# Kernel optimization log

Hardware: AMD Instinct MI355X
Metric: run time of the kernel (lower is better)

The kernel has to match this reference:

```python
import jax, jax.numpy as jnp
import numpy as np

DEPTH = 10
WIDTH = 128
DIM = 2
N = 1_048_576


def setup_inputs() -> dict:
    key = jax.random.key(0)
    ks = jax.random.split(key, 14)
    x = jax.random.normal(ks[0], (N, DIM), jnp.float32)

    # Orthogonal init for the invertible 1x1 convs (QR of a random matrix),
    # matching Invertible1x1Conv.__init__.
    rng = np.random.default_rng(0)
    conv_w = np.stack([np.linalg.qr(rng.standard_normal((DIM, DIM)))[0]
                       for _ in range(DEPTH)]).astype(np.float32)

    def nrm(k, shape, sc=0.1):
        return sc * jax.random.normal(k, shape, jnp.float32)

    return dict(
        x=x,
        an_scale=jnp.exp(nrm(ks[1], (DEPTH, DIM))),          # outer actnorm, positive
        an_bias=nrm(ks[2], (DEPTH, DIM)),
        conv_w=jnp.asarray(conv_w),                           # [D, 2, 2]
        fc1_w=nrm(ks[3], (DEPTH, WIDTH, DIM // 2), 1.0),      # Linear(1, 128)
        fc1_b=nrm(ks[4], (DEPTH, WIDTH)),
        an1_scale=jnp.exp(nrm(ks[5], (DEPTH, WIDTH))),
        an1_bias=nrm(ks[6], (DEPTH, WIDTH)),
        fc2_w=nrm(ks[7], (DEPTH, WIDTH, WIDTH)),              # Linear(128, 128)
        fc2_b=nrm(ks[8], (DEPTH, WIDTH)),
        an2_scale=jnp.exp(nrm(ks[9], (DEPTH, WIDTH))),
        an2_bias=nrm(ks[10], (DEPTH, WIDTH)),
        fc3_w=nrm(ks[11], (DEPTH, DIM, WIDTH)),               # Linear(128, 2)
        fc3_b=nrm(ks[12], (DEPTH, DIM)),
        log_scale_factor=nrm(ks[13], (DEPTH, DIM)),
    )


def reference(x, an_scale, an_bias, conv_w, fc1_w, fc1_b, an1_scale, an1_bias,
              fc2_w, fc2_b, an2_scale, an2_bias, fc3_w, fc3_b, log_scale_factor):
    z = x
    logdet = jnp.zeros((x.shape[0],), x.dtype)
    half = DIM // 2
    for i in range(DEPTH):  # fixed depth=10, structurally distinct params
        # --- Actnorm ---
        z = (z - an_bias[i]) / an_scale[i]
        logdet = logdet - jnp.sum(jnp.log(jnp.abs(an_scale[i])))
        # --- Invertible 1x1 conv ---
        logdet = logdet + jnp.linalg.slogdet(conv_w[i])[1]
        z = z @ conv_w[i].T
        # --- Affine coupling (inner actnorms are already initialized) ---
        z_a, z_b = z[:, :half], z[:, half:]
        h = jax.nn.relu((z_b @ fc1_w[i].T + fc1_b[i] - an1_bias[i]) / an1_scale[i])
        h = jax.nn.relu((h @ fc2_w[i].T + fc2_b[i] - an2_bias[i]) / an2_scale[i])
        h = (h @ fc3_w[i].T + fc3_b[i]) * jnp.exp(log_scale_factor[i])  # [N, 2]
        t = h[:, 0::2]                         # [N, 1]
        s = jax.nn.sigmoid(h[:, 1::2] + 2.0)   # [N, 1]
        z = jnp.concatenate([s * z_a + t, z_b], axis=1)
        logdet = logdet + jnp.sum(jnp.log(s), axis=1)
    return z, logdet
```

## Files before the change

kernel.cpp:

```cpp
#include <hip/hip_runtime.h>
#include <math.h>


constexpr int kDepth = 10;
constexpr int kWidth = 128;
constexpr float kVMin = -24.0f;
constexpr float kVMax =  24.0f;

__global__ void prep_kernel(
    const float* __restrict__ an_scale, const float* __restrict__ an_bias,
    const float* __restrict__ conv_w,
    const float* __restrict__ fc1_w, const float* __restrict__ fc1_b,
    const float* __restrict__ an1_scale, const float* __restrict__ an1_bias,
    const float* __restrict__ fc2_w, const float* __restrict__ fc2_b,
    const float* __restrict__ an2_scale, const float* __restrict__ an2_bias,
    const float* __restrict__ fc3_b, const float* __restrict__ lsf,
    float* __restrict__ meta, float* __restrict__ kv,
    float* __restrict__ CG, float* __restrict__ CB)
{
  __shared__ float sWT[128 * 129];
  __shared__ float sVs[128], sG[128], sB[128];
  __shared__ float sGs[128], sBs[128];
  __shared__ int   sOrd[128];

  const int l = blockIdx.x;
  const int t = threadIdx.x;

  const float* wl = fc2_w + (size_t)l * kWidth * kWidth;
#pragma unroll 8
  for (int fi = t; fi < 128 * 128; fi += 256) {
    const int k = fi >> 7, j = fi & 127;
    sWT[j * 129 + k] = wl[fi];
  }

  if (t < 128) {
    const float s1 = an1_scale[l*kWidth + t];
    const float g = fc1_w[l*kWidth + t] / s1;
    const float b = (fc1_b[l*kWidth + t] - an1_bias[l*kWidth + t]) / s1;
    float vs, sg;
    if (g > 0.0f)      { vs = -b / g; sg =  1.0f; }
    else if (g < 0.0f) { vs = -b / g; sg = -1.0f; }
    else               { vs = (b > 0.0f) ? -1e30f : 1e30f; sg = (b > 0.0f) ? 1.0f : 0.0f; }
    sG[t] = g; sB[t] = b; sVs[t] = vs;
    sGs[t] = sg * g; sBs[t] = sg * b;
  }
  __syncthreads();

  if (t < 128) {
    const float my = sVs[t];
    int r = 0;
    const float4* vs4 = (const float4*)sVs;
#pragma unroll
    for (int i4 = 0; i4 < 32; ++i4) {
      float4 o = vs4[i4];
      const int ib = i4 * 4;
      r += (o.x < my) || (o.x == my && ib + 0 < t);
      r += (o.y < my) || (o.y == my && ib + 1 < t);
      r += (o.z < my) || (o.z == my && ib + 2 < t);
      r += (o.w < my) || (o.w == my && ib + 3 < t);
    }
    sOrd[r] = t;
  }
  __syncthreads();

  if (t < 128) {
    kv[l*128 + t] = sVs[sOrd[t]];

    float cg = 0.0f;
    float cb = fc2_b[l*kWidth + t] - an2_bias[l*kWidth + t];
    const float4* g4 = (const float4*)sG;
    const float4* b4 = (const float4*)sB;
#pragma unroll
    for (int j4 = 0; j4 < 32; ++j4) {
      float4 G = g4[j4], B = b4[j4];
      const int j = j4 * 4;
      float w0 = sWT[(j + 0) * 129 + t];
      float w1 = sWT[(j + 1) * 129 + t];
      float w2 = sWT[(j + 2) * 129 + t];
      float w3 = sWT[(j + 3) * 129 + t];
      if (G.x < 0.0f) { cg = fmaf(G.x, w0, cg); cb = fmaf(B.x, w0, cb); }
      if (G.y < 0.0f) { cg = fmaf(G.y, w1, cg); cb = fmaf(B.y, w1, cb); }
      if (G.z < 0.0f) { cg = fmaf(G.z, w2, cg); cb = fmaf(B.z, w2, cb); }
      if (G.w < 0.0f) { cg = fmaf(G.w, w3, cg); cb = fmaf(B.w, w3, cb); }
    }

    const size_t base = (size_t)l * 129 * 128;
    int4 J = ((const int4*)sOrd)[0];
    float w0 = sWT[J.x * 129 + t];
    float w1 = sWT[J.y * 129 + t];
    float w2 = sWT[J.z * 129 + t];
    float w3 = sWT[J.w * 129 + t];
#pragma unroll 1
    for (int c = 0; c < 32; ++c) {
      const int4 Jc = J;
      const float v0 = w0, v1 = w1, v2 = w2, v3 = w3;
      if (c + 1 < 32) {
        J = ((const int4*)sOrd)[c + 1];
        w0 = sWT[J.x * 129 + t];
        w1 = sWT[J.y * 129 + t];
        w2 = sWT[J.z * 129 + t];
        w3 = sWT[J.w * 129 + t];
      }
      const int p = c * 4;
      CG[base + (size_t)(p + 0) * 128 + t] = cg;
      CB[base + (size_t)(p + 0) * 128 + t] = cb;
      cg = fmaf(sGs[Jc.x], v0, cg); cb = fmaf(sBs[Jc.x], v0, cb);
      CG[base + (size_t)(p + 1) * 128 + t] = cg;
      CB[base + (size_t)(p + 1) * 128 + t] = cb;
      cg = fmaf(sGs[Jc.y], v1, cg); cb = fmaf(sBs[Jc.y], v1, cb);
      CG[base + (size_t)(p + 2) * 128 + t] = cg;
      CB[base + (size_t)(p + 2) * 128 + t] = cb;
      cg = fmaf(sGs[Jc.z], v2, cg); cb = fmaf(sBs[Jc.z], v2, cb);
      CG[base + (size_t)(p + 3) * 128 + t] = cg;
      CB[base + (size_t)(p + 3) * 128 + t] = cb;
      cg = fmaf(sGs[Jc.w], v3, cg); cb = fmaf(sBs[Jc.w], v3, cb);
    }
    CG[base + (size_t)128 * 128 + t] = cg;
    CB[base + (size_t)128 * 128 + t] = cb;
  }

  if (t == 0) {
    meta[16 + l*4 + 0] = expf(lsf[l*2 + 0]);
    meta[16 + l*4 + 1] = expf(lsf[l*2 + 1]);
    meta[16 + l*4 + 2] = fc3_b[l*2 + 0];
    meta[16 + l*4 + 3] = fc3_b[l*2 + 1];

    const float sx = an_scale[l*2+0], sy = an_scale[l*2+1];
    const float bx = an_bias[l*2+0],  by = an_bias[l*2+1];
    const float* cw = conv_w + l*4;
    const float m00 = cw[0]/sx, m01 = cw[1]/sy;
    const float m10 = cw[2]/sx, m11 = cw[3]/sy;
    meta[64 + l*8 + 0] = m00;
    meta[64 + l*8 + 1] = m01;
    meta[64 + l*8 + 2] = m10;
    meta[64 + l*8 + 3] = m11;
    meta[64 + l*8 + 4] = -(m00*bx + m01*by);
    meta[64 + l*8 + 5] = -(m10*bx + m11*by);
  }
  if (l == 0 && t == 0) {
    float cst = 0.0f;
    for (int i = 0; i < kDepth; ++i) {
      cst -= logf(fabsf(an_scale[i*2+0]));
      cst -= logf(fabsf(an_scale[i*2+1]));
      const float* cw = conv_w + i * 4;
      float det = cw[0]*cw[3] - cw[1]*cw[2];
      cst += logf(fabsf(det));
    }
    meta[0] = cst;
  }
}

__global__ __launch_bounds__(256) void table_kernel(
    const float* __restrict__ an2_scale,
    const float* __restrict__ fc3_w,
    const float* __restrict__ meta, const float* __restrict__ kv,
    const float* __restrict__ CG, const float* __restrict__ CB,
    int tabN, float4* __restrict__ tab)
{
  __shared__ float sKz[128], sKw[128], sKv[128];
  __shared__ int   sP[64];

  const int bpl   = tabN >> 6;
  const int l     = blockIdx.x / bpl;
  const int node0 = (blockIdx.x % bpl) * 64;
  const int t     = threadIdx.x;
  const float dv  = (kVMax - kVMin) / (float)(tabN - 1);

  if (t < 128) {
    const float si = 1.0f / an2_scale[l*kWidth + t];
    sKz[t] = fc3_w[l*2*kWidth + t] * si;
    sKw[t] = fc3_w[l*2*kWidth + kWidth + t] * si;
    sKv[t] = kv[l*128 + t];
  }
  __syncthreads();

  if (t < 64) {
    const float v = kVMin + dv * (float)(node0 + t);
    int p = 0;
    const float4* kv4 = (const float4*)sKv;
#pragma unroll
    for (int m = 0; m < 32; ++m) {
      float4 K = kv4[m];
      p += (K.x < v) + (K.y < v) + (K.z < v) + (K.w < v);
    }
    sP[t] = p;
  }
  __syncthreads();

  const int node = t >> 2, kq = t & 3;
  const int p = sP[node];
  const float v = kVMin + dv * (float)(node0 + node);

  const float4* cg4 = (const float4*)(CG + ((size_t)l*129 + p) * 128 + kq*32);
  const float4* cb4 = (const float4*)(CB + ((size_t)l*129 + p) * 128 + kq*32);
  const float4* kz4 = (const float4*)sKz + kq*8;
  const float4* kw4 = (const float4*)sKw + kq*8;

  float o0 = 0.f, o1 = 0.f, p0 = 0.f, p1 = 0.f;
#pragma unroll
  for (int c = 0; c < 8; ++c) {
    float4 G = cg4[c], B = cb4[c], Z = kz4[c], W = kw4[c];
    float raw, h, dd;
    raw = fmaf(v, G.x, B.x); h = fmaxf(raw, 0.f); dd = (raw > 0.f) ? G.x : 0.f;
    o0 = fmaf(h, Z.x, o0); o1 = fmaf(h, W.x, o1); p0 = fmaf(dd, Z.x, p0); p1 = fmaf(dd, W.x, p1);
    raw = fmaf(v, G.y, B.y); h = fmaxf(raw, 0.f); dd = (raw > 0.f) ? G.y : 0.f;
    o0 = fmaf(h, Z.y, o0); o1 = fmaf(h, W.y, o1); p0 = fmaf(dd, Z.y, p0); p1 = fmaf(dd, W.y, p1);
    raw = fmaf(v, G.z, B.z); h = fmaxf(raw, 0.f); dd = (raw > 0.f) ? G.z : 0.f;
    o0 = fmaf(h, Z.z, o0); o1 = fmaf(h, W.z, o1); p0 = fmaf(dd, Z.z, p0); p1 = fmaf(dd, W.z, p1);
    raw = fmaf(v, G.w, B.w); h = fmaxf(raw, 0.f); dd = (raw > 0.f) ? G.w : 0.f;
    o0 = fmaf(h, Z.w, o0); o1 = fmaf(h, W.w, o1); p0 = fmaf(dd, Z.w, p0); p1 = fmaf(dd, W.w, p1);
  }

  o0 += __shfl_xor(o0, 1); o0 += __shfl_xor(o0, 2);
  o1 += __shfl_xor(o1, 1); o1 += __shfl_xor(o1, 2);
  p0 += __shfl_xor(p0, 1); p0 += __shfl_xor(p0, 2);
  p1 += __shfl_xor(p1, 1); p1 += __shfl_xor(p1, 2);

  if (kq == 0) {
    const float E0  = meta[16 + l*4 + 0];
    const float E1  = meta[16 + l*4 + 1];
    const float b30 = meta[16 + l*4 + 2];
    const float b31 = meta[16 + l*4 + 3];
    tab[(size_t)l * tabN + node0 + node] =
        make_float4((o0 + b30) * E0, p0 * E0, (o1 + b31) * E1, p1 * E1);
  }
}

__global__ __launch_bounds__(1024) void flow_apply_kernel(
    const float* __restrict__ x,
    const float4* __restrict__ tab, const float* __restrict__ meta,
    int tabN,
    float* __restrict__ out_z, float* __restrict__ out_ld, int n)
{
  __shared__ float2 sTU[2][1024];
  __shared__ float2 sDT[2][1024];

  const int t = threadIdx.x;
  const int base = blockIdx.x * 4096;

  int   sid[4];
  bool  ok[4];
  float2 z[4];
  float ldv[4];
  const float ldc = meta[0];
#pragma unroll
  for (int c = 0; c < 4; ++c) {
    sid[c] = base + c * 1024 + t;
    ok[c] = sid[c] < n;
    z[c] = ok[c] ? reinterpret_cast<const float2*>(x)[sid[c]] : make_float2(0.f, 0.f);
    ldv[c] = ldc;
  }

  const float dv = (kVMax - kVMin) / (float)(tabN - 1);
  const float inv_dv = (float)(tabN - 1) / (kVMax - kVMin);
  const float offv = -kVMin * inv_dv;
  const float qmax = (float)(tabN - 1);
  constexpr float kLog2e = 1.44269504088896340736f;
  constexpr float kLn2   = 0.69314718055994530942f;

  if (t < tabN) {
    float4 e = tab[t];
    sTU[0][t] = make_float2(e.x, e.z);
    sDT[0][t] = make_float2(e.y, e.w);
  }
  __syncthreads();

  int cur = 0;
#pragma unroll 1
  for (int i = 0; i < kDepth; ++i) {
    float4 en = make_float4(0.f, 0.f, 0.f, 0.f);
    if (i + 1 < kDepth && t < tabN)
      en = tab[(size_t)(i + 1) * tabN + t];

    const float m00 = meta[64 + i*8 + 0], m01 = meta[64 + i*8 + 1];
    const float m10 = meta[64 + i*8 + 2], m11 = meta[64 + i*8 + 3];
    const float q0  = meta[64 + i*8 + 4], q1  = meta[64 + i*8 + 5];
    const float2* tu = sTU[cur];
    const float2* dt = sDT[cur];

#pragma unroll
    for (int c = 0; c < 4; ++c) {
      const float na = fmaf(m00, z[c].x, fmaf(m01, z[c].y, q0));
      const float nb = fmaf(m10, z[c].x, fmaf(m11, z[c].y, q1));
      float xq = fmaf(nb, inv_dv, offv);
      xq = fminf(fmaxf(xq, 0.0f), qmax);
      const int qn = (int)(xq + 0.5f);
      const float2 e  = tu[qn];
      const float2 de = dt[qn];
      const float vn = fmaf((float)qn, dv, kVMin);
      const float f = nb - vn;
      const float tt = fmaf(f, de.x, e.x);
      const float uu = fmaf(f, de.y, e.y);
      const float arg = uu + 2.0f;
      const float ev = __builtin_amdgcn_exp2f(arg * -kLog2e);
      const float den = 1.0f + ev;
      const float s = __builtin_amdgcn_rcpf(den);
      ldv[c] = fmaf(-kLn2, __builtin_amdgcn_logf(den), ldv[c]);
      z[c].x = fmaf(s, na, tt);
      z[c].y = nb;
    }

    __syncthreads();
    if (i + 1 < kDepth && t < tabN) {
      sTU[cur ^ 1][t] = make_float2(en.x, en.z);
      sDT[cur ^ 1][t] = make_float2(en.y, en.w);
    }
    __syncthreads();
    cur ^= 1;
  }

#pragma unroll
  for (int c = 0; c < 4; ++c) {
    if (ok[c]) {
      reinterpret_cast<float2*>(out_z)[sid[c]] = z[c];
      out_ld[sid[c]] = ldv[c];
    }
  }
}

extern "C" void kernel_launch(void* const* d_in, const int* in_sizes, int n_in,
                              void* d_out, int out_size, void* d_ws, size_t ws_size,
                              hipStream_t stream) {
  const float* x         = (const float*)d_in[0];
  const float* an_scale  = (const float*)d_in[1];
  const float* an_bias   = (const float*)d_in[2];
  const float* conv_w    = (const float*)d_in[3];
  const float* fc1_w     = (const float*)d_in[4];
  const float* fc1_b     = (const float*)d_in[5];
  const float* an1_scale = (const float*)d_in[6];
  const float* an1_bias  = (const float*)d_in[7];
  const float* fc2_w     = (const float*)d_in[8];
  const float* fc2_b     = (const float*)d_in[9];
  const float* an2_scale = (const float*)d_in[10];
  const float* an2_bias  = (const float*)d_in[11];
  const float* fc3_w     = (const float*)d_in[12];
  const float* fc3_b     = (const float*)d_in[13];
  const float* lsf       = (const float*)d_in[14];

  const int n = in_sizes[0] / 2;

  const size_t metaF = 256, kvF = (size_t)kDepth * 128;
  const size_t cF = (size_t)kDepth * 129 * 128;
  const size_t headF = metaF + kvF + 2 * cF;
  int tabN = 1024;
  while (tabN > 256 &&
         headF * 4 + (size_t)kDepth * tabN * sizeof(float4) > ws_size) {
    tabN >>= 1;
  }
  float* meta = (float*)d_ws;
  float* kv   = meta + metaF;
  float* CG   = kv + kvF;
  float* CB   = CG + cF;
  float4* tab = (float4*)(CB + cF);

  prep_kernel<<<kDepth, 256, 0, stream>>>(
      an_scale, an_bias, conv_w, fc1_w, fc1_b, an1_scale, an1_bias,
      fc2_w, fc2_b, an2_scale, an2_bias, fc3_b, lsf,
      meta, kv, CG, CB);

  table_kernel<<<kDepth * (tabN / 64), 256, 0, stream>>>(
      an2_scale, fc3_w, meta, kv, CG, CB, tabN, tab);

  const int blocks = (n + 4095) / 4096;
  flow_apply_kernel<<<blocks, 1024, 0, stream>>>(
      x, tab, meta, tabN, (float*)d_out, (float*)d_out + (size_t)2 * n, n);
}
```

Before: 45.32 us.

## Preload all layer tables into LDS with bf16-packed slopes, drop per-layer barriers

Each block now loads every depth's lookup table into shared memory once at the start, instead of double-buffering one table per layer with two barriers per layer. To fit everything in LDS, the default table resolution drops from 1024 to 512 entries, and the two slope values are packed as bf16 into a single 32-bit word. This removes the per-layer synchronisation and the staggered global loads. The cost is a coarser piecewise-linear approximation and reduced slope precision, which could hurt accuracy, plus a larger LDS footprint per block.

Result: faster. 40.38 us (-10.9%).

```diff
diff --git a/kernel.cpp b/kernel.cpp
--- a/kernel.cpp
+++ b/kernel.cpp
@@ -226,17 +226,31 @@
   }
 }
 
+__device__ __forceinline__ unsigned int pack_bf16(float a, float b) {
+  unsigned int ua = __float_as_uint(a);
+  unsigned int ub = __float_as_uint(b);
+  ua = (ua + 0x7FFFu + ((ua >> 16) & 1u)) >> 16;
+  ub = (ub + 0x7FFFu + ((ub >> 16) & 1u)) >> 16;
+  return ua | (ub << 16);
+}
+
 __global__ __launch_bounds__(1024) void flow_apply_kernel(
     const float* __restrict__ x,
     const float4* __restrict__ tab, const float* __restrict__ meta,
     int tabN,
     float* __restrict__ out_z, float* __restrict__ out_ld, int n)
 {
-  __shared__ float2 sTU[2][1024];
-  __shared__ float2 sDT[2][1024];
+  __shared__ float2       sTU[kDepth * 512];
+  __shared__ unsigned int sPK[kDepth * 512];
 
   const int t = threadIdx.x;
   const int base = blockIdx.x * 4096;
+
+  for (int j = t; j < kDepth * tabN; j += 1024) {
+    float4 e = tab[j];
+    sTU[j] = make_float2(e.x, e.z);
+    sPK[j] = pack_bf16(e.y, e.w);
+  }
 
   int   sid[4];
   bool  ok[4];
@@ -258,25 +272,15 @@
   constexpr float kLog2e = 1.44269504088896340736f;
   constexpr float kLn2   = 0.69314718055994530942f;
 
-  if (t < tabN) {
-    float4 e = tab[t];
-    sTU[0][t] = make_float2(e.x, e.z);
-    sDT[0][t] = make_float2(e.y, e.w);
-  }
-  __syncthreads();
-
-  int cur = 0;
+  __syncthreads();
+
 #pragma unroll 1
   for (int i = 0; i < kDepth; ++i) {
-    float4 en = make_float4(0.f, 0.f, 0.f, 0.f);
-    if (i + 1 < kDepth && t < tabN)
-      en = tab[(size_t)(i + 1) * tabN + t];
-
     const float m00 = meta[64 + i*8 + 0], m01 = meta[64 + i*8 + 1];
     const float m10 = meta[64 + i*8 + 2], m11 = meta[64 + i*8 + 3];
     const float q0  = meta[64 + i*8 + 4], q1  = meta[64 + i*8 + 5];
-    const float2* tu = sTU[cur];
-    const float2* dt = sDT[cur];
+    const float2* tu = sTU + i * tabN;
+    const unsigned int* pk = sPK + i * tabN;
 
 #pragma unroll
     for (int c = 0; c < 4; ++c) {
@@ -285,12 +289,14 @@
       float xq = fmaf(nb, inv_dv, offv);
       xq = fminf(fmaxf(xq, 0.0f), qmax);
       const int qn = (int)(xq + 0.5f);
-      const float2 e  = tu[qn];
-      const float2 de = dt[qn];
+      const float2 e = tu[qn];
+      const unsigned int d = pk[qn];
+      const float dt = __uint_as_float(d << 16);
+      const float du = __uint_as_float(d & 0xFFFF0000u);
       const float vn = fmaf((float)qn, dv, kVMin);
       const float f = nb - vn;
-      const float tt = fmaf(f, de.x, e.x);
-      const float uu = fmaf(f, de.y, e.y);
+      const float tt = fmaf(f, dt, e.x);
+      const float uu = fmaf(f, du, e.y);
       const float arg = uu + 2.0f;
       const float ev = __builtin_amdgcn_exp2f(arg * -kLog2e);
       const float den = 1.0f + ev;
@@ -299,14 +305,6 @@
       z[c].x = fmaf(s, na, tt);
       z[c].y = nb;
     }
-
-    __syncthreads();
-    if (i + 1 < kDepth && t < tabN) {
-      sTU[cur ^ 1][t] = make_float2(en.x, en.z);
-      sDT[cur ^ 1][t] = make_float2(en.y, en.w);
-    }
-    __syncthreads();
-    cur ^= 1;
   }
 
 #pragma unroll
@@ -342,8 +340,8 @@
   const size_t metaF = 256, kvF = (size_t)kDepth * 128;
   const size_t cF = (size_t)kDepth * 129 * 128;
   const size_t headF = metaF + kvF + 2 * cF;
-  int tabN = 1024;
-  while (tabN > 256 &&
+  int tabN = 512;
+  while (tabN > 128 &&
          headF * 4 + (size_t)kDepth * tabN * sizeof(float4) > ws_size) {
     tabN >>= 1;
   }
```
